# Kernel tuning notes

Measured on AMD Instinct MI355X. Metric: run time of the kernel, lower is better.

The kernel has to match this reference:

```python
import jax, jax.numpy as jnp
import numpy as np

B, N, DEG = 32, 1024, 8
E = B * N * DEG
NT = B * N
F_IN, HID, EDIM, NR, HD = 64, 128, 16, 16, 4
NEG = 0.2  # leaky_relu negative slope (alpha)
K1 = int(np.ceil(0.8 * N))    # 820 kept nodes per graph after pool1
K2 = int(np.ceil(0.8 * K1))   # 656 kept nodes per graph after pool2


def setup_inputs() -> dict:
    key = jax.random.key(0)
    ks = jax.random.split(key, 20)
    nrm = lambda i, shp, s=0.05: jax.random.normal(ks[i], shp, jnp.float32) * s
    x = jax.random.normal(ks[0], (NT, F_IN), jnp.float32)
    off = (jnp.arange(B) * N)[:, None]
    src = (jax.random.randint(ks[1], (B, N * DEG), 0, N) + off).reshape(-1)
    dst = (jax.random.randint(ks[2], (B, N * DEG), 0, N) + off).reshape(-1)
    edge_index = jnp.stack([src, dst]).astype(jnp.int32)
    edge_attr = jax.random.normal(ks[3], (E, EDIM), jnp.float32)
    action = jax.random.normal(ks[4], (B, NR), jnp.float32)
    return dict(
        x=x, edge_attr=edge_attr, action=action,
        W1l=nrm(5, (F_IN, HD * HID)), b1l=jnp.zeros(HD * HID),
        W1r=nrm(6, (F_IN, HD * HID)), b1r=jnp.zeros(HD * HID),
        W1e=nrm(7, (EDIM, HD * HID)), att1=nrm(8, (HD, HID)), bias1=jnp.zeros(HID),
        W2l=nrm(9, (HID, HD * HID)), b2l=jnp.zeros(HD * HID),
        W2r=nrm(10, (HID, HD * HID)), b2r=jnp.zeros(HD * HID),
        W2e=nrm(11, (EDIM, HD * HID)), att2=nrm(12, (HD, HID)), bias2=jnp.zeros(HID),
        p1=nrm(13, (HID,), 0.1), p2=nrm(14, (HID,), 0.1),
        Wf1=nrm(15, (2 * HID + NR, HID)), bf1=jnp.zeros(HID),
        Wf2=nrm(16, (HID, HID)), bf2=jnp.zeros(HID),
        Wf3=nrm(17, (HID, 1), 0.003), bf3=jnp.zeros(1),
        edge_index=edge_index,
    )


def _gatv2(x, edge_index, edge_attr, edge_mask, Wl, bl, Wr, br, We, att, bias):
    # PyG GATv2Conv, concat=False (mean over heads), eval mode (no dropout).
    src, dst = edge_index[0], edge_index[1]
    n = x.shape[0]
    xl = (x @ Wl + bl).reshape(n, HD, HID)   # source transform (x_j)
    xr = (x @ Wr + br).reshape(n, HD, HID)   # target transform (x_i)
    ef = (edge_attr @ We).reshape(-1, HD, HID)
    m = jax.nn.leaky_relu(xl[src] + xr[dst] + ef, NEG)          # [E,H,C]
    logits = jnp.where(edge_mask[:, None], (m * att).sum(-1), -1e9)  # [E,H]
    mx = jax.ops.segment_max(logits, dst, num_segments=n)
    a = jnp.exp(logits - mx[dst])
    den = jax.ops.segment_sum(a, dst, num_segments=n)
    alpha = (a / (den[dst] + 1e-16)) * edge_mask[:, None]       # softmax per dst, masked edges zeroed
    out = jax.ops.segment_sum(xl[src] * alpha[..., None], dst, num_segments=n)
    return out.mean(axis=1) + bias


def _topk(x, node_mask, p, k):
    # PyG TopKPooling: score = x@p/||p||, gate = tanh(score), keep top-k per graph.
    score = (x @ p) / (jnp.linalg.norm(p) + 1e-16)
    gate = jnp.tanh(score)
    s = jnp.where(node_mask, score, -jnp.inf).reshape(B, N)
    idx = jax.lax.top_k(s, k)[1]                                # [B,k]
    keep = jnp.zeros((B, N), bool).at[jnp.arange(B)[:, None], idx].set(True).reshape(-1)
    return x * gate[:, None], keep


def reference(x, edge_attr, action, W1l, b1l, W1r, b1r, W1e, att1, bias1,
              W2l, b2l, W2r, b2r, W2e, att2, bias2, p1, p2,
              Wf1, bf1, Wf2, bf2, Wf3, bf3, edge_index):
    src, dst = edge_index[0], edge_index[1]
    em0 = jnp.ones((E,), bool)
    h = jax.nn.relu(_gatv2(x, edge_index, edge_attr, em0,
                           W1l, b1l, W1r, b1r, W1e, att1, bias1))
    h, keep1 = _topk(h, jnp.ones((NT,), bool), p1, K1)
    em1 = keep1[src] & keep1[dst]
    h = jax.nn.relu(_gatv2(h, edge_index, edge_attr, em1,
                           W2l, b2l, W2r, b2r, W2e, att2, bias2))
    h, keep2 = _topk(h, keep1, p2, K2)
    hb = h.reshape(B, N, HID)
    mb = keep2.reshape(B, N)[..., None]
    gmx = jnp.where(mb, hb, -jnp.inf).max(axis=1)               # global max pool over kept nodes
    gav = (hb * mb).sum(axis=1) / K2                            # global mean pool (K2 kept per graph)
    z = jnp.concatenate([gmx, gav, action], axis=1)             # [B, 2*HID+NR]
    z = jax.nn.relu(z @ Wf1 + bf1)
    z = jax.nn.relu(z @ Wf2 + bf2)
    return z @ Wf3 + bf3
```

## Files before the change

### kernel.cpp

```cpp
#include <hip/hip_runtime.h>
#include <math.h>

#define NTN 32768
#define NBG 32
#define NN  1024
#define EE  262144
#define FIN 64
#define HIDC 128
#define HD  4
#define HC  512
#define EDIM 16
#define NR  16
#define KP1 820
#define KP2 656
#define NKEPT (KP1 * NBG)
#define NEGS 0.2f
#define NPB 2
#define SHIFT 10.0f

template<int K>
__global__ __launch_bounds__(256) void gemm_node3(const float* __restrict__ A,
                                                  const float* __restrict__ Wl,
                                                  const float* __restrict__ bl,
                                                  const float* __restrict__ Wr,
                                                  const float* __restrict__ br,
                                                  const float* __restrict__ gs,
                                                  const int* __restrict__ ids,
                                                  float* __restrict__ Cl,
                                                  float* __restrict__ Cr) {
    __shared__ float a_s[64][K];
    __shared__ int rid_s[64];
    __shared__ float g_s[64];
    int t = threadIdx.x;
    int rb = blockIdx.x >> 2, cg = blockIdx.x & 3;
    int row0 = rb * 64;
    if (t < 64) {
        int rid = ids ? ids[row0 + t] : (row0 + t);
        rid_s[t] = rid;
        g_s[t] = gs ? tanhf(gs[rid]) : 1.0f;
    }
    __syncthreads();
    for (int i = t; i < 64 * K; i += 256) {
        int r = i / K, k = i % K;
        a_s[r][k] = A[(size_t)rid_s[r] * K + k] * g_s[r];
    }
    __syncthreads();
    int tc = cg * 128 + (t & 63) * 2;
    int rg = (t >> 6) * 16;
    float accl0[16], accl1[16], accr0[16], accr1[16];
    float2 blv = *(const float2*)&bl[tc];
    float2 brv = *(const float2*)&br[tc];
    #pragma unroll
    for (int r = 0; r < 16; r++) { accl0[r] = blv.x; accl1[r] = blv.y; accr0[r] = brv.x; accr1[r] = brv.y; }
    for (int k = 0; k < K; k++) {
        float2 wl = *(const float2*)&Wl[(size_t)k * HC + tc];
        float2 wr = *(const float2*)&Wr[(size_t)k * HC + tc];
        #pragma unroll
        for (int r = 0; r < 16; r++) {
            float a = a_s[rg + r][k];
            accl0[r] += a * wl.x; accl1[r] += a * wl.y;
            accr0[r] += a * wr.x; accr1[r] += a * wr.y;
        }
    }
    for (int r = 0; r < 16; r++) {
        size_t base = (size_t)rid_s[rg + r] * HC + tc;
        *(float2*)&Cl[base] = make_float2(accl0[r], accl1[r]);
        *(float2*)&Cr[base] = make_float2(accr0[r], accr1[r]);
    }
}

__global__ void edge_hist(const int* __restrict__ dst, const int* __restrict__ src,
                          const int* __restrict__ keep, int* __restrict__ deg) {
    int e = blockIdx.x * 256 + threadIdx.x;
    if (e < EE) {
        if (keep && (!keep[src[e]] || !keep[dst[e]])) return;
        atomicAdd(&deg[dst[e]], 1);
    }
}

__global__ __launch_bounds__(1024) void scan_deg(const int* __restrict__ deg,
                                                 int* __restrict__ off, int* __restrict__ cur,
                                                 const float* __restrict__ p1,
                                                 const float* __restrict__ p2,
                                                 float* __restrict__ pn) {
    __shared__ int s[1024];
    int t = threadIdx.x;
    int base = t * 32;
    int local[32];
    int sum = 0;
    #pragma unroll
    for (int i = 0; i < 32; i++) { local[i] = deg[base + i]; sum += local[i]; }
    s[t] = sum;
    for (int o = 1; o < 1024; o <<= 1) {
        __syncthreads();
        int v = (t >= o) ? s[t - o] : 0;
        __syncthreads();
        s[t] += v;
    }
    __syncthreads();
    int run = s[t] - sum;
    #pragma unroll
    for (int i = 0; i < 32; i++) { off[base + i] = run; cur[base + i] = run; run += local[i]; }
    if (t == 1023) off[NTN] = s[1023];
    if (pn && t < 64) {
        float a = p1[t] * p1[t] + p1[t + 64] * p1[t + 64];
        float b = p2[t] * p2[t] + p2[t + 64] * p2[t + 64];
        #pragma unroll
        for (int sft = 32; sft; sft >>= 1) { a += __shfl_xor(a, sft, 64); b += __shfl_xor(b, sft, 64); }
        if (t == 0) { pn[0] = 1.f / (sqrtf(a) + 1e-16f); pn[1] = 1.f / (sqrtf(b) + 1e-16f); }
    }
}

__global__ void edge_scatter(const int* __restrict__ dst, const int* __restrict__ src,
                             const int* __restrict__ keep, const float* __restrict__ ea,
                             int* __restrict__ cur,
                             int* __restrict__ esrc, float* __restrict__ eaP) {
    int e = blockIdx.x * 256 + threadIdx.x;
    if (e < EE) {
        if (keep && (!keep[src[e]] || !keep[dst[e]])) return;
        int p = atomicAdd(&cur[dst[e]], 1);
        esrc[p] = src[e];
        const float4* s4 = (const float4*)(ea + (size_t)e * EDIM);
        float4* d4 = (float4*)(eaP + (size_t)p * EDIM);
        d4[0] = s4[0]; d4[1] = s4[1]; d4[2] = s4[2]; d4[3] = s4[3];
    }
}

__global__ __launch_bounds__(256) void gat_dst(
        const float* __restrict__ xl, const float* __restrict__ xr,
        const float* __restrict__ eaP, const float* __restrict__ We,
        const float* __restrict__ att, const float* __restrict__ bias,
        const float* __restrict__ pvec, const float* __restrict__ pnInv,
        const int* __restrict__ esrc, const int* __restrict__ off,
        float* __restrict__ out, float* __restrict__ score, int nblk) {
    int bid = blockIdx.x;
    int swz = (bid & 7) * (nblk >> 3) + (bid >> 3);
    int d0 = swz * NPB;
    int t = threadIdx.x;
    int w = t >> 6, lane = t & 63;
    int c = w * HIDC + lane * 2;
    __shared__ float red[NPB][HC];
    __shared__ float red2[NPB][HIDC];
    float we0[EDIM], we1[EDIM];
    #pragma unroll
    for (int k = 0; k < EDIM; k++) {
        we0[k] = We[(size_t)k * HC + c];
        we1[k] = We[(size_t)k * HC + c + 1];
    }
    float at0 = att[c], at1 = att[c + 1];

    for (int n = 0; n < NPB; n++) {
        int d = d0 + n;
        float2 xrv = *(const float2*)&xr[((size_t)d << 9) + c];
        int e0 = off[d], e1 = off[d + 1];
        float denA = 0.f, aA0 = 0.f, aA1 = 0.f;
        float denB = 0.f, aB0 = 0.f, aB1 = 0.f;
        int ei = e0;
        for (; ei + 4 <= e1; ei += 4) {
            int s[4]; float2 xv[4]; float p[4];
            #pragma unroll
            for (int j = 0; j < 4; j++) s[j] = esrc[ei + j];
            #pragma unroll
            for (int j = 0; j < 4; j++) xv[j] = *(const float2*)&xl[((size_t)s[j] << 9) + c];
            #pragma unroll
            for (int j = 0; j < 4; j++) {
                const float4* eap = (const float4*)(eaP + ((size_t)(ei + j) << 4));
                float4 E0 = eap[0], E1 = eap[1], E2 = eap[2], E3 = eap[3];
                float ev[16] = {E0.x, E0.y, E0.z, E0.w, E1.x, E1.y, E1.z, E1.w,
                                E2.x, E2.y, E2.z, E2.w, E3.x, E3.y, E3.z, E3.w};
                float ef0 = 0.f, ef1 = 0.f;
                #pragma unroll
                for (int k = 0; k < EDIM; k++) { ef0 += ev[k] * we0[k]; ef1 += ev[k] * we1[k]; }
                float v0 = xv[j].x + xrv.x + ef0; v0 = v0 > 0.f ? v0 : NEGS * v0;
                float v1 = xv[j].y + xrv.y + ef1; v1 = v1 > 0.f ? v1 : NEGS * v1;
                p[j] = v0 * at0 + v1 * at1;
            }
            #pragma unroll
            for (int sft = 32; sft; sft >>= 1) {
                #pragma unroll
                for (int j = 0; j < 4; j++) p[j] += __shfl_xor(p[j], sft, 64);
            }
            float w0 = __expf(p[0] - SHIFT);
            float w1 = __expf(p[1] - SHIFT);
            float w2 = __expf(p[2] - SHIFT);
            float w3 = __expf(p[3] - SHIFT);
            denA += w0; aA0 += w0 * xv[0].x; aA1 += w0 * xv[0].y;
            denB += w1; aB0 += w1 * xv[1].x; aB1 += w1 * xv[1].y;
            denA += w2; aA0 += w2 * xv[2].x; aA1 += w2 * xv[2].y;
            denB += w3; aB0 += w3 * xv[3].x; aB1 += w3 * xv[3].y;
        }
        for (; ei < e1; ei++) {
            int s = esrc[ei];
            const float4* eap = (const float4*)(eaP + ((size_t)ei << 4));
            float4 E0 = eap[0], E1 = eap[1], E2 = eap[2], E3 = eap[3];
            float2 xv = *(const float2*)&xl[((size_t)s << 9) + c];
            float ev[16] = {E0.x, E0.y, E0.z, E0.w, E1.x, E1.y, E1.z, E1.w,
                            E2.x, E2.y, E2.z, E2.w, E3.x, E3.y, E3.z, E3.w};
            float ef0 = 0.f, ef1 = 0.f;
            #pragma unroll
            for (int k = 0; k < EDIM; k++) { ef0 += ev[k] * we0[k]; ef1 += ev[k] * we1[k]; }
            float v0 = xv.x + xrv.x + ef0; v0 = v0 > 0.f ? v0 : NEGS * v0;
            float v1 = xv.y + xrv.y + ef1; v1 = v1 > 0.f ? v1 : NEGS * v1;
            float p = v0 * at0 + v1 * at1;
            #pragma unroll
            for (int sft = 32; sft; sft >>= 1) p += __shfl_xor(p, sft, 64);
            float wt = __expf(p - SHIFT);
            denA += wt; aA0 += wt * xv.x; aA1 += wt * xv.y;
        }
        float inv = 1.f / (denA + denB + 1e-16f);
        red[n][c] = (aA0 + aB0) * inv;
        red[n][c + 1] = (aA1 + aB1) * inv;
    }
    __syncthreads();
    {
        int n2 = t >> 7, tc = t & 127;
        float v = (red[n2][tc] + red[n2][tc + 128] + red[n2][tc + 256] + red[n2][tc + 384]) * 0.25f
                  + bias[tc];
        v = fmaxf(v, 0.f);
        out[((size_t)(d0 + n2) << 7) + tc] = v;
        red2[n2][tc] = v * pvec[tc];
    }
    __syncthreads();
    if (t < 128) {
        int n3 = t >> 6, l2 = t & 63;
        float sv = red2[n3][l2] + red2[n3][l2 + 64];
        #pragma unroll
        for (int sft = 32; sft; sft >>= 1) sv += __shfl_xor(sv, sft, 64);
        if (l2 == 0) score[d0 + n3] = sv * pnInv[0];
    }
}

__global__ __launch_bounds__(512) void topk_sel(const float* __restrict__ score,
                                                const int* __restrict__ mask, int k,
                                                int* __restrict__ keep, int* __restrict__ klist) {
    __shared__ float v[NN];
    __shared__ short id[NN];
    int g = blockIdx.x, t = threadIdx.x;
    for (int i = t; i < NN; i += 512) {
        int n = g * NN + i;
        bool mk = mask ? (mask[n] != 0) : true;
        v[i] = mk ? score[n] : -INFINITY;
        id[i] = (short)i;
    }
    __syncthreads();
    for (int kk = 2; kk <= NN; kk <<= 1) {
        for (int j = kk >> 1; j > 0; j >>= 1) {
            #pragma unroll 2
            for (int i = t; i < NN; i += 512) {
                int ixj = i ^ j;
                if (ixj > i) {
                    bool up = ((i & kk) == 0);
                    float a = v[i], b2 = v[ixj];
                    short ia = id[i], ib = id[ixj];
                    bool aFirst = (a > b2) || (a == b2 && ia < ib);
                    if (up ? !aFirst : aFirst) { v[i] = b2; v[ixj] = a; id[i] = ib; id[ixj] = ia; }
                }
            }
            __syncthreads();
        }
    }
    for (int i = t; i < NN; i += 512) {
        int kp = (i < k) ? 1 : 0;
        keep[g * NN + id[i]] = kp;
        if (klist && kp) klist[g * k + i] = g * NN + id[i];
    }
}

__global__ __launch_bounds__(512) void tail(const float* __restrict__ score,
                                            const int* __restrict__ mask,
                                            const float* __restrict__ h,
                                            const float* __restrict__ action,
                                            const float* __restrict__ Wf1, const float* __restrict__ bf1,
                                            const float* __restrict__ Wf2, const float* __restrict__ bf2,
                                            const float* __restrict__ Wf3, const float* __restrict__ bf3,
                                            float* __restrict__ out) {
    int g = blockIdx.x, t = threadIdx.x;
    __shared__ float v[NN];
    __shared__ short id[NN];
    __shared__ float gt_s[NN];
    __shared__ char kp_s[NN];
    __shared__ float smx[4][HIDC], ssm[4][HIDC];
    __shared__ float zs[2 * HIDC + NR], z1[HIDC], z2[HIDC], rr[HIDC];
    for (int i = t; i < NN; i += 512) {
        int n = g * NN + i;
        bool mk = (mask[n] != 0);
        v[i] = mk ? score[n] : -INFINITY;
        id[i] = (short)i;
        kp_s[i] = 0;
        gt_s[i] = 0.f;
    }
    __syncthreads();
    for (int kk = 2; kk <= NN; kk <<= 1) {
        for (int j = kk >> 1; j > 0; j >>= 1) {
            #pragma unroll 2
            for (int i = t; i < NN; i += 512) {
                int ixj = i ^ j;
                if (ixj > i) {
                    bool up = ((i & kk) == 0);
                    float a = v[i], b2 = v[ixj];
                    short ia = id[i], ib = id[ixj];
                    bool aFirst = (a > b2) || (a == b2 && ia < ib);
                    if (up ? !aFirst : aFirst) { v[i] = b2; v[ixj] = a; id[i] = ib; id[ixj] = ia; }
                }
            }
            __syncthreads();
        }
    }
    for (int i = t; i < NN; i += 512) {
        if (i < KP2) {
            int nid = id[i];
            kp_s[nid] = 1;
            gt_s[nid] = tanhf(score[g * NN + nid]);
        }
    }
    __syncthreads();
    int c = t & 127, ch = t >> 7;
    float mx = -INFINITY, sm = 0.f;
    for (int n = ch * 256; n < ch * 256 + 256; n++) {
        if (kp_s[n]) {
            float hv = h[(size_t)(g * NN + n) * HIDC + c] * gt_s[n];
            mx = fmaxf(mx, hv);
            sm += hv;
        }
    }
    smx[ch][c] = mx; ssm[ch][c] = sm;
    __syncthreads();
    if (t < HIDC) {
        mx = fmaxf(fmaxf(smx[0][t], smx[1][t]), fmaxf(smx[2][t], smx[3][t]));
        sm = ssm[0][t] + ssm[1][t] + ssm[2][t] + ssm[3][t];
        zs[t] = mx;
        zs[HIDC + t] = sm / (float)KP2;
        if (t < NR) zs[2 * HIDC + t] = action[g * NR + t];
    }
    __syncthreads();
    if (t < HIDC) {
        float a = bf1[t];
        for (int k = 0; k < 2 * HIDC + NR; k++) a += zs[k] * Wf1[(size_t)k * HIDC + t];
        z1[t] = fmaxf(a, 0.f);
    }
    __syncthreads();
    if (t < HIDC) {
        float a = bf2[t];
        for (int k = 0; k < HIDC; k++) a += z1[k] * Wf2[(size_t)k * HIDC + t];
        z2[t] = fmaxf(a, 0.f);
        rr[t] = z2[t] * Wf3[t];
    }
    __syncthreads();
    for (int s = 64; s; s >>= 1) {
        if (t < s) rr[t] += rr[t + s];
        __syncthreads();
    }
    if (t == 0) out[g] = rr[0] + bf3[0];
}

extern "C" void kernel_launch(void* const* d_in, const int* in_sizes, int n_in,
                              void* d_out, int out_size, void* d_ws, size_t ws_size,
                              hipStream_t stream) {
    const float* x    = (const float*)d_in[0];
    const float* ea   = (const float*)d_in[1];
    const float* act  = (const float*)d_in[2];
    const float* W1l  = (const float*)d_in[3];
    const float* b1l  = (const float*)d_in[4];
    const float* W1r  = (const float*)d_in[5];
    const float* b1r  = (const float*)d_in[6];
    const float* W1e  = (const float*)d_in[7];
    const float* att1 = (const float*)d_in[8];
    const float* bias1= (const float*)d_in[9];
    const float* W2l  = (const float*)d_in[10];
    const float* b2l  = (const float*)d_in[11];
    const float* W2r  = (const float*)d_in[12];
    const float* b2r  = (const float*)d_in[13];
    const float* W2e  = (const float*)d_in[14];
    const float* att2 = (const float*)d_in[15];
    const float* bias2= (const float*)d_in[16];
    const float* p1   = (const float*)d_in[17];
    const float* p2   = (const float*)d_in[18];
    const float* Wf1  = (const float*)d_in[19];
    const float* bf1  = (const float*)d_in[20];
    const float* Wf2  = (const float*)d_in[21];
    const float* bf2  = (const float*)d_in[22];
    const float* Wf3  = (const float*)d_in[23];
    const float* bf3  = (const float*)d_in[24];
    const int*   eix  = (const int*)d_in[25];
    const int* srcA = eix;
    const int* dstA = eix + EE;

    float* ws    = (float*)d_ws;
    float* xl    = ws;
    float* xr    = xl + (size_t)NTN * HC;
    float* h     = xr + (size_t)NTN * HC;
    float* score1= h + (size_t)NTN * HIDC;
    float* score2= score1 + NTN;
    float* pn    = score2 + NTN;
    int* keep1 = (int*)(pn + 2);
    int* klist = keep1 + NTN;
    int* deg   = klist + NKEPT;
    int* off   = deg + NTN;
    int* cur   = off + NTN + 1;
    int* deg2  = cur + NTN;
    int* off2  = deg2 + NTN;
    int* cur2  = off2 + NTN + 1;
    int* esrc  = cur2 + NTN;
    int* esrc2 = esrc + EE;
    float* eaP  = (float*)(esrc2 + EE);
    float* eaP2 = eaP + (size_t)EE * EDIM;

    hipMemsetAsync(deg, 0, NTN * sizeof(int), stream);
    edge_hist<<<EE / 256, 256, 0, stream>>>(dstA, srcA, nullptr, deg);
    scan_deg<<<1, 1024, 0, stream>>>(deg, off, cur, p1, p2, pn);
    edge_scatter<<<EE / 256, 256, 0, stream>>>(dstA, srcA, nullptr, ea, cur, esrc, eaP);

    gemm_node3<FIN><<<(NTN / 64) * 4, 256, 0, stream>>>(x, W1l, b1l, W1r, b1r, nullptr, nullptr, xl, xr);
    gat_dst<<<NTN / NPB, 256, 0, stream>>>(xl, xr, eaP, W1e, att1, bias1, p1, pn, esrc, off, h, score1, NTN / NPB);

    topk_sel<<<NBG, 512, 0, stream>>>(score1, nullptr, KP1, keep1, klist);

    hipMemsetAsync(deg2, 0, NTN * sizeof(int), stream);
    edge_hist<<<EE / 256, 256, 0, stream>>>(dstA, srcA, keep1, deg2);
    scan_deg<<<1, 1024, 0, stream>>>(deg2, off2, cur2, nullptr, nullptr, nullptr);
    edge_scatter<<<EE / 256, 256, 0, stream>>>(dstA, srcA, keep1, ea, cur2, esrc2, eaP2);

    gemm_node3<HIDC><<<(NKEPT / 64) * 4, 256, 0, stream>>>(h, W2l, b2l, W2r, b2r, score1, klist, xl, xr);
    gat_dst<<<NTN / NPB, 256, 0, stream>>>(xl, xr, eaP2, W2e, att2, bias2, p2, pn + 1, esrc2, off2, h, score2, NTN / NPB);

    tail<<<NBG, 512, 0, stream>>>(score2, keep1, h, act,
                                  Wf1, bf1, Wf2, bf2, Wf3, bf3, (float*)d_out);
}
```

Before: 588.4 us.

## Reuse layer-1 CSR for layer 2 with keep masking and padded edge lists

The second CSR build (histogram, scan, scatter of edge attributes) for the pooled graph is removed. The second GAT layer now reuses the first CSR and masks edges whose source or destination was dropped, skipping dead destination nodes entirely. Per-node edge lists are padded to multiples of four with sentinel entries so the gather loop needs no remainder loop. The cost is extra reads of masked edges and keep flags in layer 2, plus a small pad-fill kernel.

```diff
diff --git a/kernel.cpp b/kernel.cpp
--- a/kernel.cpp
+++ b/kernel.cpp
@@ -17,6 +17,7 @@
 #define NEGS 0.2f
 #define NPB 2
 #define SHIFT 10.0f
+#define EPAD (EE + 3 * NTN + 64)
 
 template<int K>
 __global__ __launch_bounds__(256) void gemm_node3(const float* __restrict__ A,
@@ -69,13 +70,9 @@
     }
 }
 
-__global__ void edge_hist(const int* __restrict__ dst, const int* __restrict__ src,
-                          const int* __restrict__ keep, int* __restrict__ deg) {
+__global__ void edge_hist(const int* __restrict__ dst, int* __restrict__ deg) {
     int e = blockIdx.x * 256 + threadIdx.x;
-    if (e < EE) {
-        if (keep && (!keep[src[e]] || !keep[dst[e]])) return;
-        atomicAdd(&deg[dst[e]], 1);
-    }
+    if (e < EE) atomicAdd(&deg[dst[e]], 1);
 }
 
 __global__ __launch_bounds__(1024) void scan_deg(const int* __restrict__ deg,
@@ -89,7 +86,7 @@
     int local[32];
     int sum = 0;
     #pragma unroll
-    for (int i = 0; i < 32; i++) { local[i] = deg[base + i]; sum += local[i]; }
+    for (int i = 0; i < 32; i++) { local[i] = (deg[base + i] + 3) & ~3; sum += local[i]; }
     s[t] = sum;
     for (int o = 1; o < 1024; o <<= 1) {
         __syncthreads();
@@ -102,7 +99,7 @@
     #pragma unroll
     for (int i = 0; i < 32; i++) { off[base + i] = run; cur[base + i] = run; run += local[i]; }
     if (t == 1023) off[NTN] = s[1023];
-    if (pn && t < 64) {
+    if (t < 64) {
         float a = p1[t] * p1[t] + p1[t + 64] * p1[t + 64];
         float b = p2[t] * p2[t] + p2[t + 64] * p2[t + 64];
         #pragma unroll
@@ -112,17 +109,29 @@
 }
 
 __global__ void edge_scatter(const int* __restrict__ dst, const int* __restrict__ src,
-                             const int* __restrict__ keep, const float* __restrict__ ea,
-                             int* __restrict__ cur,
+                             const float* __restrict__ ea, int* __restrict__ cur,
                              int* __restrict__ esrc, float* __restrict__ eaP) {
     int e = blockIdx.x * 256 + threadIdx.x;
     if (e < EE) {
-        if (keep && (!keep[src[e]] || !keep[dst[e]])) return;
         int p = atomicAdd(&cur[dst[e]], 1);
         esrc[p] = src[e];
         const float4* s4 = (const float4*)(ea + (size_t)e * EDIM);
         float4* d4 = (float4*)(eaP + (size_t)p * EDIM);
         d4[0] = s4[0]; d4[1] = s4[1]; d4[2] = s4[2]; d4[3] = s4[3];
+    }
+}
+
+__global__ void pad_fill(const int* __restrict__ cur, const int* __restrict__ off,
+                         int* __restrict__ esrc, float* __restrict__ eaP) {
+    int d = blockIdx.x * 256 + threadIdx.x;
+    if (d < NTN) {
+        int p0 = cur[d], p1 = off[d + 1];
+        float4 z = make_float4(0.f, 0.f, 0.f, 0.f);
+        for (int p = p0; p < p1; p++) {
+            esrc[p] = -1;
+            float4* d4 = (float4*)(eaP + (size_t)p * EDIM);
+            d4[0] = z; d4[1] = z; d4[2] = z; d4[3] = z;
+        }
     }
 }
 
@@ -132,6 +141,7 @@
         const float* __restrict__ att, const float* __restrict__ bias,
         const float* __restrict__ pvec, const float* __restrict__ pnInv,
         const int* __restrict__ esrc, const int* __restrict__ off,
+        const int* __restrict__ keep,
         float* __restrict__ out, float* __restrict__ score, int nblk) {
     int bid = blockIdx.x;
     int swz = (bid & 7) * (nblk >> 3) + (bid >> 3);
@@ -144,68 +154,60 @@
     float we0[EDIM], we1[EDIM];
     #pragma unroll
     for (int k = 0; k < EDIM; k++) {
-        we0[k] = We[(size_t)k * HC + c];
-        we1[k] = We[(size_t)k * HC + c + 1];
+        we0[k] = We[k * HC + c];
+        we1[k] = We[k * HC + c + 1];
     }
     float at0 = att[c], at1 = att[c + 1];
+    const float* xlc = xl + c;
 
     for (int n = 0; n < NPB; n++) {
         int d = d0 + n;
-        float2 xrv = *(const float2*)&xr[((size_t)d << 9) + c];
-        int e0 = off[d], e1 = off[d + 1];
         float denA = 0.f, aA0 = 0.f, aA1 = 0.f;
         float denB = 0.f, aB0 = 0.f, aB1 = 0.f;
-        int ei = e0;
-        for (; ei + 4 <= e1; ei += 4) {
-            int s[4]; float2 xv[4]; float p[4];
-            #pragma unroll
-            for (int j = 0; j < 4; j++) s[j] = esrc[ei + j];
-            #pragma unroll
-            for (int j = 0; j < 4; j++) xv[j] = *(const float2*)&xl[((size_t)s[j] << 9) + c];
-            #pragma unroll
-            for (int j = 0; j < 4; j++) {
-                const float4* eap = (const float4*)(eaP + ((size_t)(ei + j) << 4));
-                float4 E0 = eap[0], E1 = eap[1], E2 = eap[2], E3 = eap[3];
-                float ev[16] = {E0.x, E0.y, E0.z, E0.w, E1.x, E1.y, E1.z, E1.w,
-                                E2.x, E2.y, E2.z, E2.w, E3.x, E3.y, E3.z, E3.w};
-                float ef0 = 0.f, ef1 = 0.f;
+        bool live = (keep == nullptr) || (keep[d] != 0);
+        if (live) {
+            float2 xrv = *(const float2*)&xr[((size_t)d << 9) + c];
+            int e0 = __builtin_amdgcn_readfirstlane(off[d]);
+            int e1 = __builtin_amdgcn_readfirstlane(off[d + 1]);
+            for (int ei = e0; ei < e1; ei += 4) {
+                int s[4]; float msk[4]; float2 xv[4]; float p[4];
                 #pragma unroll
-                for (int k = 0; k < EDIM; k++) { ef0 += ev[k] * we0[k]; ef1 += ev[k] * we1[k]; }
-                float v0 = xv[j].x + xrv.x + ef0; v0 = v0 > 0.f ? v0 : NEGS * v0;
-                float v1 = xv[j].y + xrv.y + ef1; v1 = v1 > 0.f ? v1 : NEGS * v1;
-                p[j] = v0 * at0 + v1 * at1;
+                for (int j = 0; j < 4; j++) {
+                    int sv = esrc[ei + j];
+                    int sc = sv < 0 ? 0 : sv;
+                    float mk = (sv >= 0) ? 1.f : 0.f;
+                    if (keep && sv >= 0 && !keep[sc]) mk = 0.f;
+                    s[j] = sc; msk[j] = mk;
+                }
+                #pragma unroll
+                for (int j = 0; j < 4; j++) xv[j] = *(const float2*)&xlc[(size_t)s[j] << 9];
+                #pragma unroll
+                for (int j = 0; j < 4; j++) {
+                    const float* eap = eaP + (size_t)(ei + j) * EDIM;
+                    float ef0 = 0.f, ef1 = 0.f;
+                    #pragma unroll
+                    for (int k = 0; k < EDIM; k++) {
+                        float e = eap[k];
+                        ef0 += e * we0[k]; ef1 += e * we1[k];
+                    }
+                    float v0 = xv[j].x + xrv.x + ef0; v0 = v0 > 0.f ? v0 : NEGS * v0;
+                    float v1 = xv[j].y + xrv.y + ef1; v1 = v1 > 0.f ? v1 : NEGS * v1;
+                    p[j] = v0 * at0 + v1 * at1;
+                }
+                #pragma unroll
+                for (int sft = 32; sft; sft >>= 1) {
+                    #pragma unroll
+                    for (int j = 0; j < 4; j++) p[j] += __shfl_xor(p[j], sft, 64);
+                }
+                float w0 = msk[0] * __expf(p[0] - SHIFT);
+                float w1 = msk[1] * __expf(p[1] - SHIFT);
+                float w2 = msk[2] * __expf(p[2] - SHIFT);
+                float w3 = msk[3] * __expf(p[3] - SHIFT);
+                denA += w0; aA0 += w0 * xv[0].x; aA1 += w0 * xv[0].y;
+                denB += w1; aB0 += w1 * xv[1].x; aB1 += w1 * xv[1].y;
+                denA += w2; aA0 += w2 * xv[2].x; aA1 += w2 * xv[2].y;
+                denB += w3; aB0 += w3 * xv[3].x; aB1 += w3 * xv[3].y;
             }
-            #pragma unroll
-            for (int sft = 32; sft; sft >>= 1) {
-                #pragma unroll
-                for (int j = 0; j < 4; j++) p[j] += __shfl_xor(p[j], sft, 64);
-            }
-            float w0 = __expf(p[0] - SHIFT);
-            float w1 = __expf(p[1] - SHIFT);
-            float w2 = __expf(p[2] - SHIFT);
-            float w3 = __expf(p[3] - SHIFT);
-            denA += w0; aA0 += w0 * xv[0].x; aA1 += w0 * xv[0].y;
-            denB += w1; aB0 += w1 * xv[1].x; aB1 += w1 * xv[1].y;
-            denA += w2; aA0 += w2 * xv[2].x; aA1 += w2 * xv[2].y;
-            denB += w3; aB0 += w3 * xv[3].x; aB1 += w3 * xv[3].y;
-        }
-        for (; ei < e1; ei++) {
-            int s = esrc[ei];
-            const float4* eap = (const float4*)(eaP + ((size_t)ei << 4));
-            float4 E0 = eap[0], E1 = eap[1], E2 = eap[2], E3 = eap[3];
-            float2 xv = *(const float2*)&xl[((size_t)s << 9) + c];
-            float ev[16] = {E0.x, E0.y, E0.z, E0.w, E1.x, E1.y, E1.z, E1.w,
-                            E2.x, E2.y, E2.z, E2.w, E3.x, E3.y, E3.z, E3.w};
-            float ef0 = 0.f, ef1 = 0.f;
-            #pragma unroll
-            for (int k = 0; k < EDIM; k++) { ef0 += ev[k] * we0[k]; ef1 += ev[k] * we1[k]; }
-            float v0 = xv.x + xrv.x + ef0; v0 = v0 > 0.f ? v0 : NEGS * v0;
-            float v1 = xv.y + xrv.y + ef1; v1 = v1 > 0.f ? v1 : NEGS * v1;
-            float p = v0 * at0 + v1 * at1;
-            #pragma unroll
-            for (int sft = 32; sft; sft >>= 1) p += __shfl_xor(p, sft, 64);
-            float wt = __expf(p - SHIFT);
-            denA += wt; aA0 += wt * xv.x; aA1 += wt * xv.y;
         }
         float inv = 1.f / (denA + denB + 1e-16f);
         red[n][c] = (aA0 + aB0) * inv;
@@ -397,31 +399,22 @@
     int* deg   = klist + NKEPT;
     int* off   = deg + NTN;
     int* cur   = off + NTN + 1;
-    int* deg2  = cur + NTN;
-    int* off2  = deg2 + NTN;
-    int* cur2  = off2 + NTN + 1;
-    int* esrc  = cur2 + NTN;
-    int* esrc2 = esrc + EE;
-    float* eaP  = (float*)(esrc2 + EE);
-    float* eaP2 = eaP + (size_t)EE * EDIM;
+    int* esrc  = cur + NTN;
+    float* eaP  = (float*)(esrc + EPAD);
 
     hipMemsetAsync(deg, 0, NTN * sizeof(int), stream);
-    edge_hist<<<EE / 256, 256, 0, stream>>>(dstA, srcA, nullptr, deg);
+    edge_hist<<<EE / 256, 256, 0, stream>>>(dstA, deg);
     scan_deg<<<1, 1024, 0, stream>>>(deg, off, cur, p1, p2, pn);
-    edge_scatter<<<EE / 256, 256, 0, stream>>>(dstA, srcA, nullptr, ea, cur, esrc, eaP);
+    edge_scatter<<<EE / 256, 256, 0, stream>>>(dstA, srcA, ea, cur, esrc, eaP);
+    pad_fill<<<NTN / 256, 256, 0, stream>>>(cur, off, esrc, eaP);
 
     gemm_node3<FIN><<<(NTN / 64) * 4, 256, 0, stream>>>(x, W1l, b1l, W1r, b1r, nullptr, nullptr, xl, xr);
-    gat_dst<<<NTN / NPB, 256, 0, stream>>>(xl, xr, eaP, W1e, att1, bias1, p1, pn, esrc, off, h, score1, NTN / NPB);
+    gat_dst<<<NTN / NPB, 256, 0, stream>>>(xl, xr, eaP, W1e, att1, bias1, p1, pn, esrc, off, nullptr, h, score1, NTN / NPB);
 
     topk_sel<<<NBG, 512, 0, stream>>>(score1, nullptr, KP1, keep1, klist);
 
-    hipMemsetAsync(deg2, 0, NTN * sizeof(int), stream);
-    edge_hist<<<EE / 256, 256, 0, stream>>>(dstA, srcA, keep1, deg2);
-    scan_deg<<<1, 1024, 0, stream>>>(deg2, off2, cur2, nullptr, nullptr, nullptr);
-    edge_scatter<<<EE / 256, 256, 0, stream>>>(dstA, srcA, keep1, ea, cur2, esrc2, eaP2);
-
     gemm_node3<HIDC><<<(NKEPT / 64) * 4, 256, 0, stream>>>(h, W2l, b2l, W2r, b2r, score1, klist, xl, xr);
-    gat_dst<<<NTN / NPB, 256, 0, stream>>>(xl, xr, eaP2, W2e, att2, bias2, p2, pn + 1, esrc2, off2, h, score2, NTN / NPB);
+    gat_dst<<<NTN / NPB, 256, 0, stream>>>(xl, xr, eaP, W2e, att2, bias2, p2, pn + 1, esrc, off, keep1, h, score2, NTN / NPB);
 
     tail<<<NBG, 512, 0, stream>>>(score2, keep1, h, act,
                                   Wf1, bf1, Wf2, bf2, Wf3, bf3, (float*)d_out);
```

New measurement: 600.6 us. 1.02x slower.
